# Kernel optimization log

Hardware: AMD Instinct MI355X
Metric: run time of the kernel (lower is better)

The kernel has to match this reference:

```python
import jax, jax.numpy as jnp
import numpy as np

NUM_BINS = 23
SIGMA_RATIO = 0.5
SMOOTH_NR = 1e-07
SMOOTH_DR = 1e-07

BIN_CENTERS = jnp.linspace(0.0, 1.0, NUM_BINS)  # [bins]
_sigma = jnp.mean(BIN_CENTERS[1:] - BIN_CENTERS[:-1]) * SIGMA_RATIO
PRETERM = 1.0 / (2.0 * _sigma ** 2)


def setup_inputs() -> dict:
    key = jax.random.key(0)
    k1, k2 = jax.random.split(key)
    shape = (4, 1, 96, 96, 96)
    pred = jax.random.uniform(k1, shape, dtype=jnp.float32)
    target = jax.random.uniform(k2, shape, dtype=jnp.float32)
    return {"pred": pred, "target": target}


def _parzen(img):
    # img: [B, ...] -> weight [B, N, bins], probability [B, 1, bins]
    img = jnp.clip(img, 0.0, 1.0)
    img = img.reshape(img.shape[0], -1, 1)  # [B, N, 1]
    weight = jnp.exp(-PRETERM * (img - BIN_CENTERS[None, None, :]) ** 2)  # [B, N, bins]
    weight = weight / jnp.sum(weight, axis=-1, keepdims=True)
    probability = jnp.mean(weight, axis=-2, keepdims=True)  # [B, 1, bins]
    return weight, probability


def reference(pred, target):
    wa, pa = _parzen(pred)    # wa: [B, N, bins]
    wb, pb = _parzen(target)
    n = wa.shape[1]
    # joint histogram: [B, bins, bins]
    pab = jnp.einsum('bni,bnj->bij', wa, wb) / n
    # marginal product: [B, bins, bins]
    papb = jnp.einsum('bki,bkj->bij', pa, pb)
    mi = jnp.sum(pab * jnp.log((pab + SMOOTH_NR) / (papb + SMOOTH_DR) + SMOOTH_DR), axis=(1, 2))
    return -jnp.mean(mi)
```

## Files before the change

kernel.cpp:

```cpp
#include <hip/hip_runtime.h>
#include <math.h>


#define NBINS   23
#define NCELLS  529
#define NBATCH  4
#define NVOX    884736
#define PBLK    432
#define RPB     16
#define RBLK    (PBLK / RPB)
#define RTOT    (RBLK * NBATCH)
#define RS      72
#define IMGB    (24 * RS * 2)
#define WREG    (2 * IMGB)
#define SMEMB   (4 * WREG + 2048)

typedef float    vf4  __attribute__((ext_vector_type(4)));
typedef _Float16 h8   __attribute__((ext_vector_type(8)));
typedef float    f16v __attribute__((ext_vector_type(16)));

#define G1 0.13533528f
#define G2 3.3546263e-4f
#define G3 1.5229979e-8f

__device__ __forceinline__ float window7(float x, int& i0, float* w)
{
    x = fminf(fmaxf(x, 0.0f), 1.0f);
    int ka = (int)floorf(fmaf(x, 22.0f, 0.5f));
    i0 = min(max(ka - 3, 0), 16);
    float v  = fmaf((float)(i0 + 3), -(1.0f / 22.0f), x);
    float W0 = __expf(-968.0f * v * v);
    float R  = __expf(88.0f * v);
    float Ri = __builtin_amdgcn_rcpf(R);
    float R2 = R * R,   R3 = R2 * R;
    float R2i = Ri * Ri, R3i = R2i * Ri;
    w[0] = W0 * (R3i * G3);
    w[1] = W0 * (R2i * G2);
    w[2] = W0 * (Ri  * G1);
    w[3] = W0;
    w[4] = W0 * (R   * G1);
    w[5] = W0 * (R2  * G2);
    w[6] = W0 * (R3  * G3);
    return ((w[0] + w[6]) + (w[1] + w[5])) + ((w[2] + w[4]) + w[3]);
}

__global__ __launch_bounds__(256, 5)
void mi_mfma(const float* __restrict__ pred,
             const float* __restrict__ targ,
             float* __restrict__ partial,
             double* __restrict__ pab64,
             int* __restrict__ counter)
{
    __shared__ __align__(16) char smem[SMEMB];

    if (blockIdx.x == 0 && blockIdx.y == 0) {
        for (int c = threadIdx.x; c < NBATCH * NCELLS; c += 256)
            pab64[c] = 0.0;
        if (threadIdx.x == 0) *counter = 0;
    }

    const int p    = blockIdx.x;
    const int b    = blockIdx.y;
    const int wv   = threadIdx.x >> 6;
    const int lane = threadIdx.x & 63;
    const int m    = lane & 31;
    const int h    = lane >> 5;

    char* wbase = smem + wv * WREG;
    _Float16* Aimg = (_Float16*)wbase;
    _Float16* Bimg = (_Float16*)(wbase + IMGB);

    const size_t base = (size_t)b * NVOX + (size_t)p * 2048 + (size_t)wv * 512
                      + (size_t)lane * 8;
    const vf4* __restrict__ px4 = (const vf4*)(pred + base);
    const vf4* __restrict__ py4 = (const vf4*)(targ + base);
    vf4 xa = px4[0], xb = px4[1], ya = py4[0], yb = py4[1];
    float xs[8] = {xa.x, xa.y, xa.z, xa.w, xb.x, xb.y, xb.z, xb.w};
    float ys[8] = {ya.x, ya.y, ya.z, ya.w, yb.x, yb.y, yb.z, yb.w};

    f16v acc = {};

    #pragma unroll
    for (int c = 0; c < 8; ++c) {
        vf4 z = {0.f, 0.f, 0.f, 0.f};
        #pragma unroll
        for (int it = 0; it < 6; ++it)
            *(vf4*)(wbase + (it * 64 + lane) * 16) = z;
        if (lane < 48)
            *(vf4*)(wbase + (384 + lane) * 16) = z;

        int ia, ja;
        float wa[7], wb[7];
        float sa = window7(xs[c], ia, wa);
        float sb = window7(ys[c], ja, wb);
        float inv = __builtin_amdgcn_rcpf(sa * sb);

        #pragma unroll
        for (int t = 0; t < 7; ++t) {
            Aimg[(ia + t) * RS + lane] = (_Float16)(wa[t] * inv);
            Bimg[(ja + t) * RS + lane] = (_Float16)wb[t];
        }

        #pragma unroll
        for (int s = 0; s < 4; ++s) {
            h8 Af = *(const h8*)(Aimg + m * RS + 16 * s + 8 * h);
            h8 Bf = *(const h8*)(Bimg + m * RS + 16 * s + 8 * h);
            acc = __builtin_amdgcn_mfma_f32_32x32x16_f16(Af, Bf, acc, 0, 0, 0);
        }
    }

    float* tile = (float*)wbase;
    #pragma unroll
    for (int r = 0; r < 16; ++r) {
        int row = (r & 3) + 8 * (r >> 2) + 4 * h;
        tile[row * 33 + m] = acc[r];
    }
    __syncthreads();
    for (int c = threadIdx.x; c < NCELLS; c += 256) {
        int i = c / NBINS, j = c % NBINS;
        float s = 0.0f;
        #pragma unroll
        for (int w = 0; w < 4; ++w)
            s += ((const float*)(smem + w * WREG))[i * 33 + j];
        partial[((size_t)(b * PBLK + p)) * NCELLS + c] = s;
    }
}

__global__ __launch_bounds__(256)
void mi_reduce_final(const float* __restrict__ partial,
                     double* __restrict__ pab64,
                     int* __restrict__ counter,
                     float* __restrict__ out)
{
    __shared__ double s_pab[NCELLS];
    __shared__ double s_pa[NBINS];
    __shared__ double s_pb[NBINS];
    __shared__ double s_red[4];
    __shared__ int s_last;

    const int g = blockIdx.x;
    const int b = blockIdx.y;
    const int t = threadIdx.x;
    const float* __restrict__ src =
        partial + ((size_t)b * PBLK + (size_t)g * RPB) * NCELLS;

    double a0 = 0.0, a1 = 0.0, a2 = 0.0;
    #pragma unroll
    for (int p = 0; p < RPB; ++p) {
        const float* __restrict__ row = src + (size_t)p * NCELLS;
        a0 += (double)row[t];
        a1 += (double)row[256 + t];
        if (t < NCELLS - 512) a2 += (double)row[512 + t];
    }
    atomicAdd(&pab64[b * NCELLS + t],       a0);
    atomicAdd(&pab64[b * NCELLS + 256 + t], a1);
    if (t < NCELLS - 512) atomicAdd(&pab64[b * NCELLS + 512 + t], a2);

    __syncthreads();
    if (t == 0) {
        __threadfence();
        s_last = (atomicAdd(counter, 1) == RTOT - 1);
    }
    __syncthreads();
    if (!s_last) return;

    double total = 0.0;
    for (int bb = 0; bb < NBATCH; ++bb) {
        for (int c = t; c < NCELLS; c += 256)
            s_pab[c] = __hip_atomic_load(&pab64[bb * NCELLS + c],
                                         __ATOMIC_RELAXED,
                                         __HIP_MEMORY_SCOPE_AGENT)
                       * (1.0 / (double)NVOX);
        __syncthreads();
        if (t < NBINS) {
            double r = 0.0, cl = 0.0;
            for (int j = 0; j < NBINS; ++j) {
                r  += s_pab[t * NBINS + j];
                cl += s_pab[j * NBINS + t];
            }
            s_pa[t] = r; s_pb[t] = cl;
        }
        __syncthreads();
        double tt = 0.0;
        for (int c = t; c < NCELLS; c += 256) {
            double pv   = s_pab[c];
            double papb = s_pa[c / NBINS] * s_pb[c % NBINS];
            tt += pv * log((pv + 1e-7) / (papb + 1e-7) + 1e-7);
        }
        #pragma unroll
        for (int off = 32; off > 0; off >>= 1) tt += __shfl_down(tt, off, 64);
        if ((t & 63) == 0) s_red[t >> 6] = tt;
        __syncthreads();
        if (t == 0) total += s_red[0] + s_red[1] + s_red[2] + s_red[3];
        __syncthreads();
    }
    if (t == 0) out[0] = (float)(-total * 0.25);
}

extern "C" void kernel_launch(void* const* d_in, const int* in_sizes, int n_in,
                              void* d_out, int out_size, void* d_ws, size_t ws_size,
                              hipStream_t stream)
{
    const float* pred = (const float*)d_in[0];
    const float* targ = (const float*)d_in[1];
    float* out = (float*)d_out;
    char* ws = (char*)d_ws;

    const size_t off_pab64 =
        ((size_t)NBATCH * PBLK * NCELLS * 4 + 255) & ~(size_t)255;

    float*  partial = (float*)ws;
    double* pab64   = (double*)(ws + off_pab64);
    int*    counter = (int*)(ws + off_pab64 + NBATCH * NCELLS * sizeof(double));

    mi_mfma<<<dim3(PBLK, NBATCH), 256, 0, stream>>>(pred, targ, partial,
                                                    pab64, counter);
    mi_reduce_final<<<dim3(RBLK, NBATCH), 256, 0, stream>>>(partial, pab64,
                                                            counter, out);
}
```

Measured before the change: 107.2 us.

## Fuse partial reduction and final MI into main kernel via atomic group counters

Removes the separate reduce kernel launch. Each group of 16 blocks uses an atomic counter so the last-finishing block reduces that group's partials into double accumulators, and a second counter picks the very last block to compute the MI value. Zeroing of the accumulators and counters moves to a hipMemsetAsync before the launch. This trades one kernel launch for a memset node, plus a serialized tail in the last blocks and atomic overhead.

```diff
diff --git a/kernel.cpp b/kernel.cpp
--- a/kernel.cpp
+++ b/kernel.cpp
@@ -9,7 +9,7 @@
 #define PBLK    432
 #define RPB     16
 #define RBLK    (PBLK / RPB)
-#define RTOT    (RBLK * NBATCH)
+#define NGRP    (RBLK * NBATCH)
 #define RS      72
 #define IMGB    (24 * RS * 2)
 #define WREG    (2 * IMGB)
@@ -49,15 +49,11 @@
              const float* __restrict__ targ,
              float* __restrict__ partial,
              double* __restrict__ pab64,
-             int* __restrict__ counter)
+             int* __restrict__ gcnt,
+             float* __restrict__ out)
 {
     __shared__ __align__(16) char smem[SMEMB];
-
-    if (blockIdx.x == 0 && blockIdx.y == 0) {
-        for (int c = threadIdx.x; c < NBATCH * NCELLS; c += 256)
-            pab64[c] = 0.0;
-        if (threadIdx.x == 0) *counter = 0;
-    }
+    __shared__ int s_task;
 
     const int p    = blockIdx.x;
     const int b    = blockIdx.y;
@@ -122,79 +118,96 @@
         #pragma unroll
         for (int w = 0; w < 4; ++w)
             s += ((const float*)(smem + w * WREG))[i * 33 + j];
-        partial[((size_t)(b * PBLK + p)) * NCELLS + c] = s;
-    }
-}
-
-__global__ __launch_bounds__(256)
-void mi_reduce_final(const float* __restrict__ partial,
-                     double* __restrict__ pab64,
-                     int* __restrict__ counter,
-                     float* __restrict__ out)
-{
-    __shared__ double s_pab[NCELLS];
-    __shared__ double s_pa[NBINS];
-    __shared__ double s_pb[NBINS];
-    __shared__ double s_red[4];
-    __shared__ int s_last;
-
-    const int g = blockIdx.x;
-    const int b = blockIdx.y;
-    const int t = threadIdx.x;
-    const float* __restrict__ src =
-        partial + ((size_t)b * PBLK + (size_t)g * RPB) * NCELLS;
-
-    double a0 = 0.0, a1 = 0.0, a2 = 0.0;
-    #pragma unroll
-    for (int p = 0; p < RPB; ++p) {
-        const float* __restrict__ row = src + (size_t)p * NCELLS;
-        a0 += (double)row[t];
-        a1 += (double)row[256 + t];
-        if (t < NCELLS - 512) a2 += (double)row[512 + t];
-    }
-    atomicAdd(&pab64[b * NCELLS + t],       a0);
-    atomicAdd(&pab64[b * NCELLS + 256 + t], a1);
-    if (t < NCELLS - 512) atomicAdd(&pab64[b * NCELLS + 512 + t], a2);
-
-    __syncthreads();
-    if (t == 0) {
+        __hip_atomic_store(&partial[((size_t)(b * PBLK + p)) * NCELLS + c], s,
+                           __ATOMIC_RELAXED, __HIP_MEMORY_SCOPE_AGENT);
+    }
+
+    __syncthreads();
+    if (threadIdx.x == 0) {
         __threadfence();
-        s_last = (atomicAdd(counter, 1) == RTOT - 1);
-    }
-    __syncthreads();
-    if (!s_last) return;
-
-    double total = 0.0;
-    for (int bb = 0; bb < NBATCH; ++bb) {
-        for (int c = t; c < NCELLS; c += 256)
-            s_pab[c] = __hip_atomic_load(&pab64[bb * NCELLS + c],
-                                         __ATOMIC_RELAXED,
-                                         __HIP_MEMORY_SCOPE_AGENT)
-                       * (1.0 / (double)NVOX);
-        __syncthreads();
-        if (t < NBINS) {
-            double r = 0.0, cl = 0.0;
-            for (int j = 0; j < NBINS; ++j) {
-                r  += s_pab[t * NBINS + j];
-                cl += s_pab[j * NBINS + t];
+        const int grp = b * RBLK + p / RPB;
+        int old = __hip_atomic_fetch_add(&gcnt[grp], 1, __ATOMIC_ACQ_REL,
+                                         __HIP_MEMORY_SCOPE_AGENT);
+        s_task = (old == RPB - 1) ? grp : -1;
+    }
+    __syncthreads();
+    if (s_task < 0) return;
+
+    {
+        const int grp = s_task;
+        const int rb  = grp / RBLK;
+        const int g   = grp % RBLK;
+        const int t   = threadIdx.x;
+        const float* __restrict__ src =
+            partial + ((size_t)rb * PBLK + (size_t)g * RPB) * NCELLS;
+
+        double a0 = 0.0, a1 = 0.0, a2 = 0.0;
+        #pragma unroll
+        for (int pr = 0; pr < RPB; ++pr) {
+            const float* __restrict__ row = src + (size_t)pr * NCELLS;
+            a0 += (double)__hip_atomic_load(&row[t], __ATOMIC_RELAXED,
+                                            __HIP_MEMORY_SCOPE_AGENT);
+            a1 += (double)__hip_atomic_load(&row[256 + t], __ATOMIC_RELAXED,
+                                            __HIP_MEMORY_SCOPE_AGENT);
+            if (t < NCELLS - 512)
+                a2 += (double)__hip_atomic_load(&row[512 + t], __ATOMIC_RELAXED,
+                                                __HIP_MEMORY_SCOPE_AGENT);
+        }
+        atomicAdd(&pab64[rb * NCELLS + t],       a0);
+        atomicAdd(&pab64[rb * NCELLS + 256 + t], a1);
+        if (t < NCELLS - 512) atomicAdd(&pab64[rb * NCELLS + 512 + t], a2);
+    }
+
+    __syncthreads();
+    if (threadIdx.x == 0) {
+        __threadfence();
+        int old = __hip_atomic_fetch_add(&gcnt[NGRP], 1, __ATOMIC_ACQ_REL,
+                                         __HIP_MEMORY_SCOPE_AGENT);
+        s_task = (old == NGRP - 1) ? 1 : -1;
+    }
+    __syncthreads();
+    if (s_task < 0) return;
+
+    {
+        double* s_pab = (double*)smem;
+        double* s_pa  = (double*)(smem + 4240);
+        double* s_pb  = (double*)(smem + 4432);
+        double* s_red = (double*)(smem + 4624);
+        const int t = threadIdx.x;
+
+        double total = 0.0;
+        for (int bb = 0; bb < NBATCH; ++bb) {
+            for (int c = t; c < NCELLS; c += 256)
+                s_pab[c] = __hip_atomic_load(&pab64[bb * NCELLS + c],
+                                             __ATOMIC_RELAXED,
+                                             __HIP_MEMORY_SCOPE_AGENT)
+                           * (1.0 / (double)NVOX);
+            __syncthreads();
+            if (t < NBINS) {
+                double r = 0.0, cl = 0.0;
+                for (int j = 0; j < NBINS; ++j) {
+                    r  += s_pab[t * NBINS + j];
+                    cl += s_pab[j * NBINS + t];
+                }
+                s_pa[t] = r; s_pb[t] = cl;
             }
-            s_pa[t] = r; s_pb[t] = cl;
-        }
-        __syncthreads();
-        double tt = 0.0;
-        for (int c = t; c < NCELLS; c += 256) {
-            double pv   = s_pab[c];
-            double papb = s_pa[c / NBINS] * s_pb[c % NBINS];
-            tt += pv * log((pv + 1e-7) / (papb + 1e-7) + 1e-7);
-        }
-        #pragma unroll
-        for (int off = 32; off > 0; off >>= 1) tt += __shfl_down(tt, off, 64);
-        if ((t & 63) == 0) s_red[t >> 6] = tt;
-        __syncthreads();
-        if (t == 0) total += s_red[0] + s_red[1] + s_red[2] + s_red[3];
-        __syncthreads();
-    }
-    if (t == 0) out[0] = (float)(-total * 0.25);
+            __syncthreads();
+            double tt = 0.0;
+            for (int c = t; c < NCELLS; c += 256) {
+                double pv   = s_pab[c];
+                double papb = s_pa[c / NBINS] * s_pb[c % NBINS];
+                tt += pv * log((pv + 1e-7) / (papb + 1e-7) + 1e-7);
+            }
+            #pragma unroll
+            for (int off = 32; off > 0; off >>= 1)
+                tt += __shfl_down(tt, off, 64);
+            if ((t & 63) == 0) s_red[t >> 6] = tt;
+            __syncthreads();
+            if (t == 0) total += s_red[0] + s_red[1] + s_red[2] + s_red[3];
+            __syncthreads();
+        }
+        if (t == 0) out[0] = (float)(-total * 0.25);
+    }
 }
 
 extern "C" void kernel_launch(void* const* d_in, const int* in_sizes, int n_in,
@@ -206,15 +219,11 @@
     float* out = (float*)d_out;
     char* ws = (char*)d_ws;
 
-    const size_t off_pab64 =
-        ((size_t)NBATCH * PBLK * NCELLS * 4 + 255) & ~(size_t)255;
-
-    float*  partial = (float*)ws;
-    double* pab64   = (double*)(ws + off_pab64);
-    int*    counter = (int*)(ws + off_pab64 + NBATCH * NCELLS * sizeof(double));
-
+    double* pab64   = (double*)ws;
+    int*    gcnt    = (int*)(ws + 16928);
+    float*  partial = (float*)(ws + 32768);
+
+    (void)hipMemsetAsync(ws, 0, 17408, stream);
     mi_mfma<<<dim3(PBLK, NBATCH), 256, 0, stream>>>(pred, targ, partial,
-                                                    pab64, counter);
-    mi_reduce_final<<<dim3(RBLK, NBATCH), 256, 0, stream>>>(partial, pab64,
-                                                            counter, out);
+                                                    pab64, gcnt, out);
 }
```

Measured after the change: 176.2 us. 1.64x slower.

## Write aligned 8-bin weight chunks and load MFMA operands with transposing LDS reads

Applied to the files above, without the earlier changes.

Replaces the 7-tap window plus full LDS zeroing and per-element scattered fp16 stores with a 16-tap window snapped to one of three aligned 8-bin offsets. Each lane now writes three 16-byte vector chunks, zeros included, so the separate zeroing pass goes away. The MFMA operands are read back with ds_read_b64_tr_b16 transposing loads from a lane-major layout. The cost is more exp evaluations per voxel and explicit waitcnt/sched barriers that may serialize LDS and MFMA work. The epilogue still reads the per-wave region as a 33-stride float tile, which needs 4.3KB per wave, while the new wave region is 8KB.

```diff
diff --git a/kernel.cpp b/kernel.cpp
--- a/kernel.cpp
+++ b/kernel.cpp
@@ -10,12 +10,12 @@
 #define RPB     16
 #define RBLK    (PBLK / RPB)
 #define RTOT    (RBLK * NBATCH)
-#define RS      72
-#define IMGB    (24 * RS * 2)
-#define WREG    (2 * IMGB)
-#define SMEMB   (4 * WREG + 2048)
+#define IMGB3   4096
+#define WREG    (2 * IMGB3)
+#define SMEMB   (4 * WREG)
 
 typedef float    vf4  __attribute__((ext_vector_type(4)));
+typedef _Float16 h4   __attribute__((ext_vector_type(4)));
 typedef _Float16 h8   __attribute__((ext_vector_type(8)));
 typedef float    f16v __attribute__((ext_vector_type(16)));
 
@@ -23,25 +23,48 @@
 #define G2 3.3546263e-4f
 #define G3 1.5229979e-8f
 
-__device__ __forceinline__ float window7(float x, int& i0, float* w)
+__device__ __forceinline__ float window16(float x, int& i0, float* w)
 {
     x = fminf(fmaxf(x, 0.0f), 1.0f);
     int ka = (int)floorf(fmaf(x, 22.0f, 0.5f));
-    i0 = min(max(ka - 3, 0), 16);
-    float v  = fmaf((float)(i0 + 3), -(1.0f / 22.0f), x);
-    float W0 = __expf(-968.0f * v * v);
-    float R  = __expf(88.0f * v);
-    float Ri = __builtin_amdgcn_rcpf(R);
-    float R2 = R * R,   R3 = R2 * R;
-    float R2i = Ri * Ri, R3i = R2i * Ri;
-    w[0] = W0 * (R3i * G3);
-    w[1] = W0 * (R2i * G2);
-    w[2] = W0 * (Ri  * G1);
-    w[3] = W0;
-    w[4] = W0 * (R   * G1);
-    w[5] = W0 * (R2  * G2);
-    w[6] = W0 * (R3  * G3);
-    return ((w[0] + w[6]) + (w[1] + w[5])) + ((w[2] + w[4]) + w[3]);
+    i0 = (ka >= 11) ? ((ka >= 19) ? 16 : 8) : 0;
+    #pragma unroll
+    for (int q = 0; q < 4; ++q) {
+        float vq = fmaf((float)(i0 + 4 * q), -(1.0f / 22.0f), x);
+        float W0 = __expf(-968.0f * vq * vq);
+        float R  = __expf(88.0f * vq);
+        float p  = W0;
+        w[4 * q + 0] = p;
+        p *= R;  w[4 * q + 1] = p * G1;
+        p *= R;  w[4 * q + 2] = p * G2;
+        p *= R;  w[4 * q + 3] = p * G3;
+    }
+    float s06  = ((w[0] + w[1]) + (w[2] + w[3])) + ((w[4] + w[5]) + w[6]);
+    float s714 = ((w[7] + w[8]) + (w[9] + w[10]))
+               + ((w[11] + w[12]) + (w[13] + w[14]));
+    float s = s06;
+    if (i0 < 16)  s += s714;
+    if (i0 == 0)  s += w[15];
+    return s;
+}
+
+__device__ __forceinline__ void write_col3(char* img, int lane, const float* w,
+                                           float scale, int i0)
+{
+    h8 lo, hi;
+    #pragma unroll
+    for (int t = 0; t < 8; ++t) {
+        lo[t] = (_Float16)(w[t] * scale);
+        hi[t] = (_Float16)(w[t + 8] * scale);
+    }
+    h8 z = {};
+    h8 c0 = (i0 == 0)  ? lo : z;
+    h8 c1 = (i0 == 0)  ? hi : ((i0 == 8) ? lo : z);
+    h8 c2 = (i0 == 16) ? lo : ((i0 == 8) ? hi : z);
+    const int aw = lane * 32;
+    *(h8*)(img + aw)        = c0;
+    *(h8*)(img + aw + 16)   = c1;
+    *(h8*)(img + aw + 2048) = c2;
 }
 
 __global__ __launch_bounds__(256, 5)
@@ -67,8 +90,8 @@
     const int h    = lane >> 5;
 
     char* wbase = smem + wv * WREG;
-    _Float16* Aimg = (_Float16*)wbase;
-    _Float16* Bimg = (_Float16*)(wbase + IMGB);
+    char* Aimg  = wbase;
+    char* Bimg  = wbase + IMGB3;
 
     const size_t base = (size_t)b * NVOX + (size_t)p * 2048 + (size_t)wv * 512
                       + (size_t)lane * 8;
@@ -78,33 +101,43 @@
     float xs[8] = {xa.x, xa.y, xa.z, xa.w, xb.x, xb.y, xb.z, xb.w};
     float ys[8] = {ya.x, ya.y, ya.z, ya.w, yb.x, yb.y, yb.z, yb.w};
 
+    const int g = lane >> 4;
+    const uint32_t aA = (uint32_t)(uintptr_t)Aimg
+                      + (uint32_t)((g & 1) * 2048 + (g >> 1) * 256
+                                   + (lane & 15) * 8);
+    const uint32_t aB = aA + IMGB3;
+
     f16v acc = {};
 
     #pragma unroll
     for (int c = 0; c < 8; ++c) {
-        vf4 z = {0.f, 0.f, 0.f, 0.f};
-        #pragma unroll
-        for (int it = 0; it < 6; ++it)
-            *(vf4*)(wbase + (it * 64 + lane) * 16) = z;
-        if (lane < 48)
-            *(vf4*)(wbase + (384 + lane) * 16) = z;
-
-        int ia, ja;
-        float wa[7], wb[7];
-        float sa = window7(xs[c], ia, wa);
-        float sb = window7(ys[c], ja, wb);
+        int iA, iB;
+        float wA[16], wB[16];
+        float sa = window16(xs[c], iA, wA);
+        float sb = window16(ys[c], iB, wB);
         float inv = __builtin_amdgcn_rcpf(sa * sb);
 
-        #pragma unroll
-        for (int t = 0; t < 7; ++t) {
-            Aimg[(ia + t) * RS + lane] = (_Float16)(wa[t] * inv);
-            Bimg[(ja + t) * RS + lane] = (_Float16)wb[t];
-        }
+        write_col3(Aimg, lane, wA, inv,  iA);
+        write_col3(Bimg, lane, wB, 1.0f, iB);
+
+        asm volatile("s_waitcnt lgkmcnt(0)" ::: "memory");
+        __builtin_amdgcn_sched_barrier(0);
 
         #pragma unroll
         for (int s = 0; s < 4; ++s) {
-            h8 Af = *(const h8*)(Aimg + m * RS + 16 * s + 8 * h);
-            h8 Bf = *(const h8*)(Bimg + m * RS + 16 * s + 8 * h);
+            h4 al, ah, bl, bh;
+            asm volatile("ds_read_b64_tr_b16 %0, %1 offset:%c2"
+                         : "=v"(al) : "v"(aA), "i"(s * 512) : "memory");
+            asm volatile("ds_read_b64_tr_b16 %0, %1 offset:%c2"
+                         : "=v"(ah) : "v"(aA), "i"(s * 512 + 128) : "memory");
+            asm volatile("ds_read_b64_tr_b16 %0, %1 offset:%c2"
+                         : "=v"(bl) : "v"(aB), "i"(s * 512) : "memory");
+            asm volatile("ds_read_b64_tr_b16 %0, %1 offset:%c2"
+                         : "=v"(bh) : "v"(aB), "i"(s * 512 + 128) : "memory");
+            asm volatile("s_waitcnt lgkmcnt(0)" ::: "memory");
+            __builtin_amdgcn_sched_barrier(0);
+            h8 Af = __builtin_shufflevector(al, ah, 0, 1, 2, 3, 4, 5, 6, 7);
+            h8 Bf = __builtin_shufflevector(bl, bh, 0, 1, 2, 3, 4, 5, 6, 7);
             acc = __builtin_amdgcn_mfma_f32_32x32x16_f16(Af, Bf, acc, 0, 0, 0);
         }
     }
```

Measured after the change: 114.8 us. 1.07x slower.
